# Optimization experiments

Measured on AMD Instinct MI355X. Metric: run time of the kernel, lower is better.

## Reference

```python
import jax, jax.numpy as jnp
import numpy as np

B, N, DIM = 2, 512, 256
H, DH = 8, 32
INNER = H * DH        # 256
EDGE_DIM = DIM        # default(edge_dim, dim)
SCALE = DH ** -0.5


def setup_inputs() -> dict:
    key = jax.random.key(0)
    ks = jax.random.split(key, 12)
    s = 0.02
    f32 = jnp.float32
    nodes = jax.random.normal(ks[0], (B, N, DIM), f32)
    edges = jax.random.normal(ks[1], (B, N, N, EDGE_DIM), f32)
    Wq  = jax.random.normal(ks[2], (DIM, INNER), f32) * s
    bq  = jax.random.normal(ks[3], (INNER,), f32) * s
    Wkv = jax.random.normal(ks[4], (DIM, 2 * INNER), f32) * s
    bkv = jax.random.normal(ks[5], (2 * INNER,), f32) * s
    We  = jax.random.normal(ks[6], (EDGE_DIM, INNER), f32) * s
    be  = jax.random.normal(ks[7], (INNER,), f32) * s
    Wo  = jax.random.normal(ks[8], (INNER, DIM), f32) * s
    bo  = jax.random.normal(ks[9], (DIM,), f32) * s
    return {"nodes": nodes, "edges": edges, "Wq": Wq, "bq": bq,
            "Wkv": Wkv, "bkv": bkv, "We": We, "be": be, "Wo": Wo, "bo": bo}


def reference(nodes, edges, Wq, bq, Wkv, bkv, We, be, Wo, bo):
    b, n, _ = nodes.shape
    # projections
    q = (nodes @ Wq + bq).reshape(b, n, H, DH).transpose(0, 2, 1, 3)   # b h i d
    kv = nodes @ Wkv + bkv
    k, v = jnp.split(kv, 2, axis=-1)
    k = k.reshape(b, n, H, DH).transpose(0, 2, 1, 3)                   # b h j d
    v = v.reshape(b, n, H, DH).transpose(0, 2, 1, 3)                   # b h j d
    e = (edges @ We + be).reshape(b, n, n, H, DH).transpose(0, 3, 1, 2, 4)  # b h i j d
    # sim = q . (k + e)  — split to avoid materializing k broadcast; same math
    sim = (jnp.einsum('bhid,bhjd->bhij', q, k)
           + jnp.einsum('bhid,bhijd->bhij', q, e)) * SCALE
    attn = jax.nn.softmax(sim, axis=-1)
    # out = attn . (v + e)
    out = (jnp.einsum('bhij,bhjd->bhid', attn, v)
           + jnp.einsum('bhij,bhijd->bhid', attn, e))
    out = out.transpose(0, 2, 1, 3).reshape(b, n, INNER)               # b n (h d)
    return out @ Wo + bo
```

## Files before the change

### kernel.cpp

```cpp
#include <hip/hip_runtime.h>
#include <hip/hip_bf16.h>
#include <stdint.h>

#define NB 2
#define NN 512
#define NDIM 256
#define NH 8
#define NDH 32
#define SCALE 0.17677669529663687f

__global__ __launch_bounds__(256) void k_proj(
    const float* __restrict__ nodes, const float* __restrict__ Wq, const float* __restrict__ bq,
    const float* __restrict__ Wkv, const float* __restrict__ bkv,
    const float* __restrict__ We, const float* __restrict__ be,
    float* __restrict__ q, float* __restrict__ k, float* __restrict__ v,
    float* __restrict__ qe, float* __restrict__ qbe)
{
    const int row0 = blockIdx.x * 2;
    const int t = threadIdx.x;
    __shared__ float xs[2][NDIM];
    __shared__ float qs[2][NDIM];
    xs[0][t] = nodes[(size_t)row0*NDIM + t];
    xs[1][t] = nodes[(size_t)(row0+1)*NDIM + t];
    __syncthreads();

    float accq0 = bq[t],        accq1 = bq[t];
    float acck0 = bkv[t],       acck1 = bkv[t];
    float accv0 = bkv[t+NDIM],  accv1 = bkv[t+NDIM];
    #pragma unroll 8
    for (int d = 0; d < NDIM; ++d) {
        const float w0 = Wq [(size_t)d*NDIM + t];
        const float w1 = Wkv[(size_t)d*2*NDIM + t];
        const float w2 = Wkv[(size_t)d*2*NDIM + t + NDIM];
        const float x0 = xs[0][d], x1 = xs[1][d];
        accq0 += x0*w0; accq1 += x1*w0;
        acck0 += x0*w1; acck1 += x1*w1;
        accv0 += x0*w2; accv1 += x1*w2;
    }
    q[(size_t)row0*NDIM + t] = accq0;  q[(size_t)(row0+1)*NDIM + t] = accq1;
    k[(size_t)row0*NDIM + t] = acck0;  k[(size_t)(row0+1)*NDIM + t] = acck1;
    v[(size_t)row0*NDIM + t] = accv0;  v[(size_t)(row0+1)*NDIM + t] = accv1;
    qs[0][t] = accq0; qs[1][t] = accq1;
    __syncthreads();

    const float* wrow = We + (size_t)t*NDIM;
    #pragma unroll
    for (int h = 0; h < NH; ++h) {
        float a0 = 0.f, a1 = 0.f, b0 = 0.f, b1 = 0.f;
        #pragma unroll
        for (int d4 = 0; d4 < NDH/4; ++d4) {
            float4 w4 = *(const float4*)(wrow + h*NDH + d4*4);
            const float* qp0 = &qs[0][h*NDH + d4*4];
            const float* qp1 = &qs[1][h*NDH + d4*4];
            a0 += qp0[0]*w4.x + qp0[1]*w4.y;
            a1 += qp0[2]*w4.z + qp0[3]*w4.w;
            b0 += qp1[0]*w4.x + qp1[1]*w4.y;
            b1 += qp1[2]*w4.z + qp1[3]*w4.w;
        }
        qe[((size_t)row0*NH + h)*NDIM + t]     = a0 + a1;
        qe[((size_t)(row0+1)*NH + h)*NDIM + t] = b0 + b1;
    }
    if (t < 2*NH) {
        const int r = t >> 3, h = t & 7;
        float a = 0.f;
        #pragma unroll 4
        for (int d = 0; d < NDH; ++d) a += qs[r][h*NDH + d]*be[h*NDH + d];
        qbe[(size_t)(row0+r)*NH + h] = a;
    }
}

__global__ __launch_bounds__(256, 4) void k_attn(
    const float* __restrict__ edges,
    const float* __restrict__ We, const float* __restrict__ be,
    const float* __restrict__ Wo, const float* __restrict__ bo,
    const float* __restrict__ q, const float* __restrict__ k, const float* __restrict__ v,
    const float* __restrict__ qe, const float* __restrict__ qbe,
    float* __restrict__ out)
{
    const int row = blockIdx.x;
    const int b = row >> 9;
    const int t = threadIdx.x;
    const int gA = t & 31, sA = t >> 5;
    const int jlB = t & 31, hB = t >> 5;
    const int hOwn = t >> 5;

    __shared__ __align__(16) float uni[2560];
    __shared__ __align__(16) float simbuf[32*9];
    __shared__ __align__(16) float pbuf[32*12];
    __shared__ float mh[8], lh[8];
    __shared__ __align__(16) float al[8];

    float* qe_s   = uni;
    float* qrow_s = uni + 2048;

    const float* Erow = edges + (size_t)row*NN*NDIM;
    const float* krow = k + (size_t)b*NN*NDIM + hB*NDH;

    float4 ea[4], eb4[4];
    {
        const float* ep0 = Erow + (size_t)sA*NDIM + gA*8;
        #pragma unroll
        for (int m = 0; m < 4; ++m) {
            ea[m]  = *(const float4*)(ep0 + (size_t)m*8*NDIM);
            eb4[m] = *(const float4*)(ep0 + (size_t)m*8*NDIM + 4);
        }
    }
    {
        const float* qp = qe + (size_t)row*(NH*NDIM) + t*8;
        float4 a0 = *(const float4*)(qp);
        float4 a1 = *(const float4*)(qp + 4);
        *(float4*)(qe_s + t*8)     = a0;
        *(float4*)(qe_s + t*8 + 4) = a1;
        qrow_s[t] = q[(size_t)row*NDIM + t];
    }
    const float qbeV = qbe[(size_t)row*NH + hB];
    float w_r[8];
    float ov_r = 0.f;
    #pragma unroll
    for (int r = 0; r < 8; ++r) w_r[r] = 0.f;
    if (t < 8) { mh[t] = -1e30f; lh[t] = 0.f; }
    __syncthreads();

    for (int jc = 0; jc < 16; ++jc) {
        const int j0 = jc*32;
        float v32_[32];
        #pragma unroll
        for (int h = 0; h < 8; ++h) {
            const float4 qa = *(const float4*)(qe_s + h*NDIM + gA*8);
            const float4 qb = *(const float4*)(qe_s + h*NDIM + gA*8 + 4);
            #pragma unroll
            for (int m = 0; m < 4; ++m) {
                v32_[m*8+h] =
                    ea[m].x*qa.x + ea[m].y*qa.y + ea[m].z*qa.z + ea[m].w*qa.w +
                    eb4[m].x*qb.x + eb4[m].y*qb.y + eb4[m].z*qb.z + eb4[m].w*qb.w;
            }
        }
        float v16_[16];
        {
            const bool bb = (gA & 16) != 0;
            #pragma unroll
            for (int i = 0; i < 16; ++i) {
                const float lo = v32_[i], hi = v32_[i+16];
                const float ot = __shfl_xor(bb ? lo : hi, 16, 64);
                v16_[i] = (bb ? hi : lo) + ot;
            }
        }
        float v8_[8];
        {
            const bool bb = (gA & 8) != 0;
            #pragma unroll
            for (int i = 0; i < 8; ++i) {
                const float lo = v16_[i], hi = v16_[i+8];
                const float ot = __shfl_xor(bb ? lo : hi, 8, 64);
                v8_[i] = (bb ? hi : lo) + ot;
            }
        }
        float v4_[4];
        {
            const bool bb = (gA & 4) != 0;
            #pragma unroll
            for (int i = 0; i < 4; ++i) {
                const float lo = v8_[i], hi = v8_[i+4];
                const float ot = __shfl_xor(bb ? lo : hi, 4, 64);
                v4_[i] = (bb ? hi : lo) + ot;
            }
        }
        float v2_[2];
        {
            const bool bb = (gA & 2) != 0;
            #pragma unroll
            for (int i = 0; i < 2; ++i) {
                const float lo = v4_[i], hi = v4_[i+2];
                const float ot = __shfl_xor(bb ? lo : hi, 2, 64);
                v2_[i] = (bb ? hi : lo) + ot;
            }
        }
        float sacc;
        {
            const bool bb = (gA & 1) != 0;
            const float lo = v2_[0], hi = v2_[1];
            const float ot = __shfl_xor(bb ? lo : hi, 1, 64);
            sacc = (bb ? hi : lo) + ot;
        }
        simbuf[(sA + (gA >> 3)*8)*9 + (gA & 7)] = sacc;
        __syncthreads();

        if (jc < 15) {
            const float* epn = Erow + (size_t)(j0 + 32 + sA)*NDIM + gA*8;
            #pragma unroll
            for (int m = 0; m < 4; ++m) {
                ea[m]  = *(const float4*)(epn + (size_t)m*8*NDIM);
                eb4[m] = *(const float4*)(epn + (size_t)m*8*NDIM + 4);
            }
        }

        {
            const int j = j0 + jlB;
            const float* kp = krow + (size_t)j*NDIM;
            const float* qp = qrow_s + hB*NDH;
            float d0=0.f,d1=0.f,d2=0.f,d3=0.f;
            #pragma unroll
            for (int u = 0; u < 8; ++u) {
                float4 kv4 = *(const float4*)(kp + u*4);
                float4 qv4 = *(const float4*)(qp + u*4);
                d0 += qv4.x*kv4.x; d1 += qv4.y*kv4.y;
                d2 += qv4.z*kv4.z; d3 += qv4.w*kv4.w;
            }
            const float sim = SCALE*(((d0+d1)+(d2+d3)) + qbeV + simbuf[jlB*9 + hB]);
            float cm = sim;
            #pragma unroll
            for (int off = 16; off >= 1; off >>= 1)
                cm = fmaxf(cm, __shfl_xor(cm, off, 64));
            const float mold = mh[hB];
            const float mnew = fmaxf(mold, cm);
            const float a_ = __expf(mold - mnew);
            const float p = __expf(sim - mnew);
            float ps = p;
            #pragma unroll
            for (int off = 16; off >= 1; off >>= 1)
                ps += __shfl_xor(ps, off, 64);
            if (jlB == 0) {
                mh[hB] = mnew;
                lh[hB] = lh[hB]*a_ + ps;
                al[hB] = a_;
            }
            pbuf[jlB*12 + hB] = p;
        }
        __syncthreads();
        {
            const float4 al0 = *(const float4*)(al);
            const float4 al1 = *(const float4*)(al + 4);
            w_r[0]*=al0.x; w_r[1]*=al0.y; w_r[2]*=al0.z; w_r[3]*=al0.w;
            w_r[4]*=al1.x; w_r[5]*=al1.y; w_r[6]*=al1.z; w_r[7]*=al1.w;
            ov_r *= al[hOwn];
            const float* eb = Erow + (size_t)j0*NDIM + t;
            const float* vb = v + ((size_t)b*NN + j0)*NDIM + t;
            #pragma unroll 8
            for (int jl = 0; jl < 32; ++jl) {
                const float ee = eb[(size_t)jl*NDIM];
                const float vv = vb[(size_t)jl*NDIM];
                const float4 p0 = *(const float4*)(pbuf + jl*12);
                const float4 p1 = *(const float4*)(pbuf + jl*12 + 4);
                const float pv = pbuf[jl*12 + hOwn];
                w_r[0] += p0.x*ee; w_r[1] += p0.y*ee; w_r[2] += p0.z*ee; w_r[3] += p0.w*ee;
                w_r[4] += p1.x*ee; w_r[5] += p1.y*ee; w_r[6] += p1.z*ee; w_r[7] += p1.w*ee;
                ov_r += pv*vv;
            }
        }
    }

    float* wfull  = uni;
    float* ovfull = uni + 2048;
    float* oibuf  = uni + 2304;
    #pragma unroll
    for (int h = 0; h < 8; ++h) wfull[h*NDIM + t] = w_r[h];
    ovfull[t] = ov_r;
    __syncthreads();
    {
        const int u = t, hu = u >> 5;
        const float linv = 1.f/lh[hu];
        const float* wrow = wfull + hu*NDIM;
        float a0=0.f,a1=0.f,a2=0.f,a3=0.f;
        #pragma unroll 2
        for (int c = 0; c < NDIM; c += 4) {
            a0 += wrow[c+0]*We[(size_t)(c+0)*NDIM + u];
            a1 += wrow[c+1]*We[(size_t)(c+1)*NDIM + u];
            a2 += wrow[c+2]*We[(size_t)(c+2)*NDIM + u];
            a3 += wrow[c+3]*We[(size_t)(c+3)*NDIM + u];
        }
        oibuf[u] = (ovfull[u] + ((a0+a1)+(a2+a3)))*linv + be[u];
    }
    __syncthreads();
    {
        const int u = t;
        float a0=bo[u],a1=0.f,a2=0.f,a3=0.f;
        #pragma unroll 2
        for (int x = 0; x < NDIM; x += 4) {
            a0 += oibuf[x+0]*Wo[(size_t)(x+0)*NDIM + u];
            a1 += oibuf[x+1]*Wo[(size_t)(x+1)*NDIM + u];
            a2 += oibuf[x+2]*Wo[(size_t)(x+2)*NDIM + u];
            a3 += oibuf[x+3]*Wo[(size_t)(x+3)*NDIM + u];
        }
        out[(size_t)row*NDIM + u] = (a0+a1)+(a2+a3);
    }
}

extern "C" void kernel_launch(void* const* d_in, const int* in_sizes, int n_in,
                              void* d_out, int out_size, void* d_ws, size_t ws_size,
                              hipStream_t stream) {
    const float* nodes = (const float*)d_in[0];
    const float* edges = (const float*)d_in[1];
    const float* Wq  = (const float*)d_in[2];
    const float* bq  = (const float*)d_in[3];
    const float* Wkv = (const float*)d_in[4];
    const float* bkv = (const float*)d_in[5];
    const float* We  = (const float*)d_in[6];
    const float* be  = (const float*)d_in[7];
    const float* Wo  = (const float*)d_in[8];
    const float* bo  = (const float*)d_in[9];
    (void)in_sizes; (void)n_in; (void)out_size; (void)ws_size;

    float* ws  = (float*)d_ws;
    float* q   = ws;
    float* k   = q  + 262144;
    float* v   = k  + 262144;
    float* qe  = v  + 262144;
    float* qbe = qe + 2097152;

    k_proj<<<dim3(NB*NN/2), dim3(256), 0, stream>>>(nodes, Wq, bq, Wkv, bkv, We, be,
                                                    q, k, v, qe, qbe);
    k_attn<<<dim3(NB*NN), dim3(256), 0, stream>>>(edges, We, be, Wo, bo,
                                                  q, k, v, qe, qbe,
                                                  (float*)d_out);
}
```

Baseline: 927.6 us.

## Split attention key range across two block halves with split-softmax merge

```diff
diff --git a/kernel.cpp b/kernel.cpp
--- a/kernel.cpp
+++ b/kernel.cpp
@@ -69,7 +69,7 @@
     }
 }
 
-__global__ __launch_bounds__(256, 4) void k_attn(
+__global__ __launch_bounds__(512, 8) void k_attn(
     const float* __restrict__ edges,
     const float* __restrict__ We, const float* __restrict__ be,
     const float* __restrict__ Wo, const float* __restrict__ bo,
@@ -80,15 +80,21 @@
     const int row = blockIdx.x;
     const int b = row >> 9;
     const int t = threadIdx.x;
-    const int gA = t & 31, sA = t >> 5;
-    const int jlB = t & 31, hB = t >> 5;
-    const int hOwn = t >> 5;
+    const int half = t >> 8;
+    const int u = t & 255;
+    const int gA = u & 31, sA = u >> 5;
+    const int jlB = u & 31, hB = u >> 5;
+    const int hOwn = u >> 5;
+    const int jbase = half * 256;
 
     __shared__ __align__(16) float uni[2560];
-    __shared__ __align__(16) float simbuf[32*9];
-    __shared__ __align__(16) float pbuf[32*12];
-    __shared__ float mh[8], lh[8];
-    __shared__ __align__(16) float al[8];
+    __shared__ __align__(16) float simbuf[2][288];
+    __shared__ __align__(16) float pbuf[2][384];
+    __shared__ __align__(16) float mh[2][8];
+    __shared__ __align__(16) float lh[2][8];
+    __shared__ __align__(16) float al[2][8];
+    __shared__ __align__(16) float a0s[8], a1s[8], linvs[8];
+    __shared__ __align__(16) float epb[2][256];
 
     float* qe_s   = uni;
     float* qrow_s = uni + 2048;
@@ -98,36 +104,39 @@
 
     float4 ea[4], eb4[4];
     {
-        const float* ep0 = Erow + (size_t)sA*NDIM + gA*8;
+        const float* ep0 = Erow + (size_t)(jbase + sA)*NDIM + gA*8;
         #pragma unroll
         for (int m = 0; m < 4; ++m) {
             ea[m]  = *(const float4*)(ep0 + (size_t)m*8*NDIM);
             eb4[m] = *(const float4*)(ep0 + (size_t)m*8*NDIM + 4);
         }
     }
-    {
+    if (t < 256) {
         const float* qp = qe + (size_t)row*(NH*NDIM) + t*8;
-        float4 a0 = *(const float4*)(qp);
-        float4 a1 = *(const float4*)(qp + 4);
-        *(float4*)(qe_s + t*8)     = a0;
-        *(float4*)(qe_s + t*8 + 4) = a1;
-        qrow_s[t] = q[(size_t)row*NDIM + t];
+        float4 A0 = *(const float4*)(qp);
+        float4 A1 = *(const float4*)(qp + 4);
+        const int sw = (t >> 2) & 1;
+        *(float4*)(qe_s + t*8 + (sw ? 4 : 0)) = A0;
+        *(float4*)(qe_s + t*8 + (sw ? 0 : 4)) = A1;
+    } else {
+        qrow_s[u] = q[(size_t)row*NDIM + u];
     }
     const float qbeV = qbe[(size_t)row*NH + hB];
     float w_r[8];
     float ov_r = 0.f;
     #pragma unroll
     for (int r = 0; r < 8; ++r) w_r[r] = 0.f;
-    if (t < 8) { mh[t] = -1e30f; lh[t] = 0.f; }
-    __syncthreads();
-
-    for (int jc = 0; jc < 16; ++jc) {
-        const int j0 = jc*32;
+    if (t < 16) { mh[t>>3][t&7] = -1e30f; lh[t>>3][t&7] = 0.f; }
+    __syncthreads();
+
+    for (int jc = 0; jc < 8; ++jc) {
+        const int j0 = jbase + jc*32;
         float v32_[32];
+        const int swr = (gA >> 2) & 1;
         #pragma unroll
         for (int h = 0; h < 8; ++h) {
-            const float4 qa = *(const float4*)(qe_s + h*NDIM + gA*8);
-            const float4 qb = *(const float4*)(qe_s + h*NDIM + gA*8 + 4);
+            const float4 qa = *(const float4*)(qe_s + h*NDIM + gA*8 + (swr ? 4 : 0));
+            const float4 qb = *(const float4*)(qe_s + h*NDIM + gA*8 + (swr ? 0 : 4));
             #pragma unroll
             for (int m = 0; m < 4; ++m) {
                 v32_[m*8+h] =
@@ -182,10 +191,10 @@
             const float ot = __shfl_xor(bb ? lo : hi, 1, 64);
             sacc = (bb ? hi : lo) + ot;
         }
-        simbuf[(sA + (gA >> 3)*8)*9 + (gA & 7)] = sacc;
+        simbuf[half][(sA + (gA >> 3)*8)*9 + (gA & 7)] = sacc;
         __syncthreads();
 
-        if (jc < 15) {
+        if (jc < 7) {
             const float* epn = Erow + (size_t)(j0 + 32 + sA)*NDIM + gA*8;
             #pragma unroll
             for (int m = 0; m < 4; ++m) {
@@ -200,18 +209,18 @@
             const float* qp = qrow_s + hB*NDH;
             float d0=0.f,d1=0.f,d2=0.f,d3=0.f;
             #pragma unroll
-            for (int u = 0; u < 8; ++u) {
-                float4 kv4 = *(const float4*)(kp + u*4);
-                float4 qv4 = *(const float4*)(qp + u*4);
+            for (int uu = 0; uu < 8; ++uu) {
+                float4 kv4 = *(const float4*)(kp + uu*4);
+                float4 qv4 = *(const float4*)(qp + uu*4);
                 d0 += qv4.x*kv4.x; d1 += qv4.y*kv4.y;
                 d2 += qv4.z*kv4.z; d3 += qv4.w*kv4.w;
             }
-            const float sim = SCALE*(((d0+d1)+(d2+d3)) + qbeV + simbuf[jlB*9 + hB]);
+            const float sim = SCALE*(((d0+d1)+(d2+d3)) + qbeV + simbuf[half][jlB*9 + hB]);
             float cm = sim;
             #pragma unroll
             for (int off = 16; off >= 1; off >>= 1)
                 cm = fmaxf(cm, __shfl_xor(cm, off, 64));
-            const float mold = mh[hB];
+            const float mold = mh[half][hB];
             const float mnew = fmaxf(mold, cm);
             const float a_ = __expf(mold - mnew);
             const float p = __expf(sim - mnew);
@@ -220,28 +229,29 @@
             for (int off = 16; off >= 1; off >>= 1)
                 ps += __shfl_xor(ps, off, 64);
             if (jlB == 0) {
-                mh[hB] = mnew;
-                lh[hB] = lh[hB]*a_ + ps;
-                al[hB] = a_;
-            }
-            pbuf[jlB*12 + hB] = p;
+                mh[half][hB] = mnew;
+                lh[half][hB] = lh[half][hB]*a_ + ps;
+                al[half][hB] = a_;
+            }
+            pbuf[half][jlB*12 + hB] = p;
         }
         __syncthreads();
         {
-            const float4 al0 = *(const float4*)(al);
-            const float4 al1 = *(const float4*)(al + 4);
+            const float4 al0 = *(const float4*)(al[half]);
+            const float4 al1 = *(const float4*)(al[half] + 4);
             w_r[0]*=al0.x; w_r[1]*=al0.y; w_r[2]*=al0.z; w_r[3]*=al0.w;
             w_r[4]*=al1.x; w_r[5]*=al1.y; w_r[6]*=al1.z; w_r[7]*=al1.w;
-            ov_r *= al[hOwn];
-            const float* eb = Erow + (size_t)j0*NDIM + t;
-            const float* vb = v + ((size_t)b*NN + j0)*NDIM + t;
+            ov_r *= al[half][hOwn];
+            const float* eb = Erow + (size_t)j0*NDIM + u;
+            const float* vb = v + ((size_t)b*NN + j0)*NDIM + u;
+            const float* pb = pbuf[half];
             #pragma unroll 8
             for (int jl = 0; jl < 32; ++jl) {
                 const float ee = eb[(size_t)jl*NDIM];
                 const float vv = vb[(size_t)jl*NDIM];
-                const float4 p0 = *(const float4*)(pbuf + jl*12);
-                const float4 p1 = *(const float4*)(pbuf + jl*12 + 4);
-                const float pv = pbuf[jl*12 + hOwn];
+                const float4 p0 = *(const float4*)(pb + jl*12);
+                const float4 p1 = *(const float4*)(pb + jl*12 + 4);
+                const float pv = pb[jl*12 + hOwn];
                 w_r[0] += p0.x*ee; w_r[1] += p0.y*ee; w_r[2] += p0.z*ee; w_r[3] += p0.w*ee;
                 w_r[4] += p1.x*ee; w_r[5] += p1.y*ee; w_r[6] += p1.z*ee; w_r[7] += p1.w*ee;
                 ov_r += pv*vv;
@@ -249,40 +259,61 @@
         }
     }
 
+    if (t < 8) {
+        const float m0 = mh[0][t], m1 = mh[1][t];
+        const float mS = fmaxf(m0, m1);
+        const float A0 = __expf(m0 - mS), A1 = __expf(m1 - mS);
+        const float l  = lh[0][t]*A0 + lh[1][t]*A1;
+        a0s[t] = A0; a1s[t] = A1; linvs[t] = 1.f/l;
+    }
+    __syncthreads();
     float* wfull  = uni;
     float* ovfull = uni + 2048;
     float* oibuf  = uni + 2304;
-    #pragma unroll
-    for (int h = 0; h < 8; ++h) wfull[h*NDIM + t] = w_r[h];
-    ovfull[t] = ov_r;
+    if (half == 0) {
+        #pragma unroll
+        for (int h = 0; h < 8; ++h) wfull[h*NDIM + u] = w_r[h]*a0s[h];
+        ovfull[u] = ov_r*a0s[hOwn];
+    }
+    __syncthreads();
+    if (half == 1) {
+        #pragma unroll
+        for (int h = 0; h < 8; ++h) wfull[h*NDIM + u] += w_r[h]*a1s[h];
+        ovfull[u] += ov_r*a1s[hOwn];
+    }
     __syncthreads();
     {
-        const int u = t, hu = u >> 5;
-        const float linv = 1.f/lh[hu];
-        const float* wrow = wfull + hu*NDIM;
+        const int hu = u >> 5;
+        const float* wrow = wfull + hu*NDIM + half*128;
+        const float* Wep  = We + (size_t)(half*128)*NDIM + u;
         float a0=0.f,a1=0.f,a2=0.f,a3=0.f;
         #pragma unroll 2
-        for (int c = 0; c < NDIM; c += 4) {
-            a0 += wrow[c+0]*We[(size_t)(c+0)*NDIM + u];
-            a1 += wrow[c+1]*We[(size_t)(c+1)*NDIM + u];
-            a2 += wrow[c+2]*We[(size_t)(c+2)*NDIM + u];
-            a3 += wrow[c+3]*We[(size_t)(c+3)*NDIM + u];
-        }
-        oibuf[u] = (ovfull[u] + ((a0+a1)+(a2+a3)))*linv + be[u];
-    }
+        for (int c = 0; c < 128; c += 4) {
+            a0 += wrow[c+0]*Wep[(size_t)(c+0)*NDIM];
+            a1 += wrow[c+1]*Wep[(size_t)(c+1)*NDIM];
+            a2 += wrow[c+2]*Wep[(size_t)(c+2)*NDIM];
+            a3 += wrow[c+3]*Wep[(size_t)(c+3)*NDIM];
+        }
+        epb[half][u] = (a0+a1)+(a2+a3);
+    }
+    __syncthreads();
+    if (half == 0) oibuf[u] = (ovfull[u] + epb[0][u] + epb[1][u])*linvs[u>>5] + be[u];
     __syncthreads();
     {
-        const int u = t;
-        float a0=bo[u],a1=0.f,a2=0.f,a3=0.f;
+        const float* oip = oibuf + half*128;
+        const float* Wop = Wo + (size_t)(half*128)*NDIM + u;
+        float a0=0.f,a1=0.f,a2=0.f,a3=0.f;
         #pragma unroll 2
-        for (int x = 0; x < NDIM; x += 4) {
-            a0 += oibuf[x+0]*Wo[(size_t)(x+0)*NDIM + u];
-            a1 += oibuf[x+1]*Wo[(size_t)(x+1)*NDIM + u];
-            a2 += oibuf[x+2]*Wo[(size_t)(x+2)*NDIM + u];
-            a3 += oibuf[x+3]*Wo[(size_t)(x+3)*NDIM + u];
-        }
-        out[(size_t)row*NDIM + u] = (a0+a1)+(a2+a3);
-    }
+        for (int x = 0; x < 128; x += 4) {
+            a0 += oip[x+0]*Wop[(size_t)(x+0)*NDIM];
+            a1 += oip[x+1]*Wop[(size_t)(x+1)*NDIM];
+            a2 += oip[x+2]*Wop[(size_t)(x+2)*NDIM];
+            a3 += oip[x+3]*Wop[(size_t)(x+3)*NDIM];
+        }
+        epb[half][u] = (a0+a1)+(a2+a3);
+    }
+    __syncthreads();
+    if (half == 0) out[(size_t)row*NDIM + u] = bo[u] + epb[0][u] + epb[1][u];
 }
 
 extern "C" void kernel_launch(void* const* d_in, const int* in_sizes, int n_in,
@@ -309,7 +340,7 @@
 
     k_proj<<<dim3(NB*NN/2), dim3(256), 0, stream>>>(nodes, Wq, bq, Wkv, bkv, We, be,
                                                     q, k, v, qe, qbe);
-    k_attn<<<dim3(NB*NN), dim3(256), 0, stream>>>(edges, We, be, Wo, bo,
+    k_attn<<<dim3(NB*NN), dim3(512), 0, stream>>>(edges, We, be, Wo, bo,
                                                   q, k, v, qe, qbe,
                                                   (float*)d_out);
 }
```

After: 1.195 ms. +28.8%, slower.
